# Kernel optimization log

Hardware: AMD Instinct MI355X
Metric: run time of the kernel (lower is better)

Reference implementation:

```python
import jax, jax.numpy as jnp
import numpy as np

D_MODEL = 1024
N_HEADS = 16
B, T = 2, 2048


def setup_inputs() -> dict:
    key = jax.random.key(0)
    ks = jax.random.split(key, 5)
    scale = 1.0 / np.sqrt(D_MODEL)
    return {
        "x": jax.random.normal(ks[0], (B, T, D_MODEL), dtype=jnp.float32),
        "W_q": jax.random.normal(ks[1], (D_MODEL, D_MODEL), dtype=jnp.float32) * scale,
        "W_k": jax.random.normal(ks[2], (D_MODEL, D_MODEL), dtype=jnp.float32) * scale,
        "W_v": jax.random.normal(ks[3], (D_MODEL, D_MODEL), dtype=jnp.float32) * scale,
        "W_o": jax.random.normal(ks[4], (D_MODEL, D_MODEL), dtype=jnp.float32) * scale,
    }


def reference(x, W_q, W_k, W_v, W_o):
    Bn, Tn, D = x.shape
    H = N_HEADS
    Dh = D // H
    # nn.Linear(x) = x @ W.T ; weights stored as [out, in]
    q = (x @ W_q.T).reshape(Bn, Tn, H, Dh).transpose(0, 2, 1, 3)  # [B,H,T,Dh]
    k = (x @ W_k.T).reshape(Bn, Tn, H, Dh).transpose(0, 2, 1, 3)
    v = (x @ W_v.T).reshape(Bn, Tn, H, Dh).transpose(0, 2, 1, 3)
    scores = jnp.einsum("bhqd,bhkd->bhqk", q, k) / np.sqrt(Dh).astype(np.float32)
    attn = jax.nn.softmax(scores, axis=-1)  # [B,H,T,T]
    out = jnp.einsum("bhqk,bhkd->bhqd", attn, v)  # [B,H,T,Dh]
    out = out.transpose(0, 2, 1, 3).reshape(Bn, Tn, D)
    return out @ W_o.T
```

## Files before the change

### kernel.cpp

```cpp
#include <hip/hip_runtime.h>
#include <stdint.h>
#include <stddef.h>


typedef __bf16  bf16x8  __attribute__((ext_vector_type(8)));
typedef __bf16  bf16x4  __attribute__((ext_vector_type(4)));
typedef float   floatx4 __attribute__((ext_vector_type(4)));

#define DEV static __device__ __forceinline__

DEV void ld_g2l16(const void* g, void* l) {
    __builtin_amdgcn_global_load_lds(
        (__attribute__((address_space(1))) void*)g,
        (__attribute__((address_space(3))) void*)l,
        16, 0, 0);
}

#define WK_SCALE 0.18033688011112042f

__global__ __launch_bounds__(256) void cvt_all(
    const float* __restrict__ x,
    const float* __restrict__ wq, const float* __restrict__ wk,
    const float* __restrict__ wv, const float* __restrict__ wo,
    __bf16* __restrict__ xb,
    __bf16* __restrict__ wqb, __bf16* __restrict__ wkb,
    __bf16* __restrict__ wvb, __bf16* __restrict__ wob)
{
    const unsigned t0 = blockIdx.x * 256u + threadIdx.x;
#pragma unroll
    for (int k = 0; k < 4; ++k) {
        unsigned u = t0 + (unsigned)k * 524288u;
        const float* src;
        __bf16* dst;
        unsigned off;
        float mul = 1.0f;
        if (u < 1048576u) {
            src = x; dst = xb; off = u;
        } else {
            unsigned u2 = u - 1048576u;
            unsigned sel = u2 >> 18;
            off = u2 & 0x3FFFFu;
            src = (sel == 0) ? wq : (sel == 1) ? wk : (sel == 2) ? wv : wo;
            dst = (sel == 0) ? wqb : (sel == 1) ? wkb : (sel == 2) ? wvb : wob;
            if (sel == 1) mul = WK_SCALE;
        }
        float4 f = *(const float4*)(src + (size_t)off * 4);
        bf16x4 o = { (__bf16)(f.x * mul), (__bf16)(f.y * mul),
                     (__bf16)(f.z * mul), (__bf16)(f.w * mul) };
        *(bf16x4*)(dst + (size_t)off * 4) = o;
    }
}

template<int BM, int NMAT, bool OUT_F32, bool TR_V, int KH>
__global__ __launch_bounds__(256) void gemm_bt(
    const __bf16* __restrict__ A,
    const __bf16* __restrict__ B0, const __bf16* __restrict__ B1,
    const __bf16* __restrict__ B2,
    void* __restrict__ C0, void* __restrict__ C1, void* __restrict__ C2)
{
    constexpr int Kd = 1024;
    constexpr int N  = 1024;
    constexpr int MI = BM / 32;
    constexpr int NA = BM / 64;
    __shared__ __bf16 As[KH][BM * 32];
    __shared__ __bf16 Bs[KH][128 * 32];

    const int t    = threadIdx.x;
    const int wid  = __builtin_amdgcn_readfirstlane(t >> 6);
    const int lane = t & 63;
    const int quad = lane >> 4;
    const int l15  = lane & 15;

    const int bx  = blockIdx.x;
    const int mat = (NMAT > 1) ? (bx >> 3) : 0;
    const int bn  = (NMAT > 1) ? (bx & 7)  : bx;
    const int bm  = blockIdx.y;
    const __bf16* Bm = (mat == 0) ? B0 : (mat == 1) ? B1 : B2;

    const __bf16* pA[NA];
    const __bf16* pB[2];
#pragma unroll
    for (int i = 0; i < NA; ++i) {
        int c    = i * 256 + t;
        int row  = c >> 2;
        int g    = (c & 3) ^ ((row >> 1) & 3);
        pA[i] = A + (size_t)(bm * BM + row) * Kd + g * 8;
    }
#pragma unroll
    for (int i = 0; i < 2; ++i) {
        int c    = i * 256 + t;
        int row  = c >> 2;
        int g    = (c & 3) ^ ((row >> 1) & 3);
        pB[i] = Bm + (size_t)(bn * 128 + row) * Kd + g * 8;
    }

    const int wm = wid >> 1;
    const int wn = wid & 1;
    const int slotr = quad ^ ((l15 >> 1) & 3);

    floatx4 acc[MI][4];
    const floatx4 z = { 0.f, 0.f, 0.f, 0.f };
#pragma unroll
    for (int i = 0; i < MI; ++i)
#pragma unroll
        for (int j = 0; j < 4; ++j) acc[i][j] = z;

    for (int kb = 0; kb < Kd; kb += 32 * KH) {
        __syncthreads();
#pragma unroll
        for (int h = 0; h < KH; ++h) {
#pragma unroll
            for (int i = 0; i < NA; ++i)
                ld_g2l16(pA[i] + kb + h * 32,
                         (char*)&As[h][0] + i * 4096 + wid * 1024);
#pragma unroll
            for (int i = 0; i < 2; ++i)
                ld_g2l16(pB[i] + kb + h * 32,
                         (char*)&Bs[h][0] + i * 4096 + wid * 1024);
        }
        __syncthreads();

#pragma unroll
        for (int h = 0; h < KH; ++h) {
            bf16x8 af[MI], bf[4];
#pragma unroll
            for (int i = 0; i < MI; ++i) {
                int rowA = wm * (BM / 2) + i * 16 + l15;
                af[i] = *(const bf16x8*)&As[h][rowA * 32 + slotr * 8];
            }
#pragma unroll
            for (int j = 0; j < 4; ++j) {
                int rowB = wn * 64 + j * 16 + l15;
                bf[j] = *(const bf16x8*)&Bs[h][rowB * 32 + slotr * 8];
            }
#pragma unroll
            for (int i = 0; i < MI; ++i)
#pragma unroll
                for (int j = 0; j < 4; ++j)
                    acc[i][j] = __builtin_amdgcn_mfma_f32_16x16x32_bf16(
                        af[i], bf[j], acc[i][j], 0, 0, 0);
        }
    }

    const int row0 = bm * BM + wm * (BM / 2);
    const int col0 = bn * 128 + wn * 64;

    if (TR_V && mat == 2) {
        __bf16* Vt = (__bf16*)C2;
        const int bq    = bm >> 4;
        const int tloc0 = (row0 & 2047) + quad * 4;
#pragma unroll
        for (int i = 0; i < MI; ++i)
#pragma unroll
            for (int j = 0; j < 4; ++j) {
                int col = col0 + j * 16 + l15;
                int hh  = col >> 6, dh = col & 63;
                bf16x4 v = { (__bf16)acc[i][j][0], (__bf16)acc[i][j][1],
                             (__bf16)acc[i][j][2], (__bf16)acc[i][j][3] };
                *(bf16x4*)(Vt + ((size_t)(bq * 16 + hh) * 64 + dh) * 2048
                              + tloc0 + i * 16) = v;
            }
    } else {
        void* Cv = (mat == 0) ? C0 : (mat == 1) ? C1 : C2;
#pragma unroll
        for (int i = 0; i < MI; ++i)
#pragma unroll
            for (int j = 0; j < 4; ++j)
#pragma unroll
                for (int r = 0; r < 4; ++r) {
                    int grow = row0 + i * 16 + quad * 4 + r;
                    int gcol = col0 + j * 16 + l15;
                    if (OUT_F32)
                        ((float*)Cv)[(size_t)grow * N + gcol] = acc[i][j][r];
                    else
                        ((__bf16*)Cv)[(size_t)grow * N + gcol] =
                            (__bf16)acc[i][j][r];
                }
    }
}

__global__ __launch_bounds__(256, 2) void flash_kernel(
    const __bf16* __restrict__ Q, const __bf16* __restrict__ K,
    const __bf16* __restrict__ Vt, __bf16* __restrict__ O)
{
    __shared__ __bf16 Qs[128 * 64];
    __shared__ __bf16 Ks[2][64 * 64];
    __shared__ __bf16 Vs[2][64 * 64];

    const int t    = threadIdx.x;
    const int wid  = __builtin_amdgcn_readfirstlane(t >> 6);
    const int half = wid >> 1;
    const int wsub = wid & 1;
    const int lane = t & 63;
    const int quad = lane >> 4;
    const int l15  = lane & 15;
    const int flat = blockIdx.y * 16 + blockIdx.x;
    const int swz  = (flat & 7) * 64 + (flat >> 3);
    const int qt   = swz & 15;
    const int bh   = swz >> 4;
    const int b    = bh >> 4, h = bh & 15;

#pragma unroll
    for (int i = 0; i < 4; ++i) {
        int c = i * 256 + t;
        int row = c >> 3;
        int g   = (c & 7) ^ (row & 7);
        ld_g2l16(Q + (size_t)(b * 2048 + qt * 128 + row) * 1024 + h * 64 + g * 8,
                 (char*)Qs + i * 4096 + wid * 1024);
    }

    const __bf16* pK[2];
    const __bf16* pV[2];
#pragma unroll
    for (int i = 0; i < 2; ++i) {
        int c = i * 256 + t;
        int srow = c >> 3;
        int sg   = (c & 7) ^ (srow & 7);
        pK[i] = K  + (size_t)(b * 2048 + srow) * 1024 + h * 64 + sg * 8;
        pV[i] = Vt + (size_t)(bh * 64 + srow) * 2048 + sg * 8;
    }

    __syncthreads();

    bf16x8 qf[4][2];
#pragma unroll
    for (int nb = 0; nb < 4; ++nb)
#pragma unroll
        for (int ks = 0; ks < 2; ++ks) {
            int row  = wsub * 64 + nb * 16 + l15;
            int slot = (ks * 4 + quad) ^ (row & 7);
            qf[nb][ks] = *(const bf16x8*)&Qs[row * 64 + slot * 8];
        }

    int koff[2];
#pragma unroll
    for (int ks = 0; ks < 2; ++ks)
        koff[ks] = l15 * 128 + (((ks * 4 + quad) ^ (l15 & 7)) << 4);
    int voff[4];
#pragma unroll
    for (int k16 = 0; k16 < 4; ++k16)
        voff[k16] = l15 * 128 + (((k16 * 2 + (quad >> 1)) ^ (l15 & 7)) << 4)
                  + (quad & 1) * 8;

    const floatx4 z = { 0.f, 0.f, 0.f, 0.f };
    floatx4 o[4][4];
#pragma unroll
    for (int nb = 0; nb < 4; ++nb)
#pragma unroll
        for (int nd = 0; nd < 4; ++nd) o[nb][nd] = z;
    float lsum[4] = { 0.f, 0.f, 0.f, 0.f };

    for (int it = 0; it < 16; ++it) {
        __syncthreads();
#pragma unroll
        for (int i = 0; i < 2; ++i) {
            ld_g2l16(pK[i] + (size_t)it * 65536,
                     (char*)Ks[0] + i * 4096 + wid * 1024);
            ld_g2l16(pK[i] + (size_t)(16 + it) * 65536,
                     (char*)Ks[1] + i * 4096 + wid * 1024);
            ld_g2l16(pV[i] + it * 64,
                     (char*)Vs[0] + i * 4096 + wid * 1024);
            ld_g2l16(pV[i] + (16 + it) * 64,
                     (char*)Vs[1] + i * 4096 + wid * 1024);
        }
        __syncthreads();

        const char* kbase = (const char*)Ks[half];
        const char* vbase = (const char*)Vs[half];
#pragma unroll
        for (int kt32 = 0; kt32 < 2; ++kt32) {
            floatx4 s[2][4];
#pragma unroll
            for (int sub = 0; sub < 2; ++sub) {
#pragma unroll
                for (int nb = 0; nb < 4; ++nb) s[sub][nb] = z;
                const int kt16 = kt32 * 2 + sub;
#pragma unroll
                for (int ks = 0; ks < 2; ++ks) {
                    bf16x8 kf = *(const bf16x8*)(kbase + kt16 * 2048
                                                 + koff[ks]);
#pragma unroll
                    for (int nb = 0; nb < 4; ++nb)
                        s[sub][nb] = __builtin_amdgcn_mfma_f32_16x16x32_bf16(
                            kf, qf[nb][ks], s[sub][nb], 0, 0, 0);
                }
            }
            bf16x8 pb8[4];
#pragma unroll
            for (int nb = 0; nb < 4; ++nb) {
#pragma unroll
                for (int sub = 0; sub < 2; ++sub) {
                    float p0 = __builtin_amdgcn_exp2f(s[sub][nb][0]);
                    float p1 = __builtin_amdgcn_exp2f(s[sub][nb][1]);
                    float p2 = __builtin_amdgcn_exp2f(s[sub][nb][2]);
                    float p3 = __builtin_amdgcn_exp2f(s[sub][nb][3]);
                    lsum[nb] += (p0 + p1) + (p2 + p3);
                    pb8[nb][sub * 4 + 0] = (__bf16)p0;
                    pb8[nb][sub * 4 + 1] = (__bf16)p1;
                    pb8[nb][sub * 4 + 2] = (__bf16)p2;
                    pb8[nb][sub * 4 + 3] = (__bf16)p3;
                }
            }
#pragma unroll
            for (int nd = 0; nd < 4; ++nd) {
                bf16x4 va0 = *(const bf16x4*)(vbase + nd * 2048
                                              + voff[kt32 * 2 + 0]);
                bf16x4 va1 = *(const bf16x4*)(vbase + nd * 2048
                                              + voff[kt32 * 2 + 1]);
                bf16x8 va8;
#pragma unroll
                for (int r = 0; r < 4; ++r) {
                    va8[r]     = va0[r];
                    va8[4 + r] = va1[r];
                }
#pragma unroll
                for (int nb = 0; nb < 4; ++nb)
                    o[nb][nd] = __builtin_amdgcn_mfma_f32_16x16x32_bf16(
                        va8, pb8[nb], o[nb][nd], 0, 0, 0);
            }
        }
    }

    __syncthreads();
    float* obuf = (wsub == 0) ? (float*)&Ks[0][0] : (float*)&Vs[0][0];
    float* lbuf = (float*)&Qs[0] + wsub * 256;
    if (half == 1) {
#pragma unroll
        for (int nb = 0; nb < 4; ++nb)
#pragma unroll
            for (int nd = 0; nd < 4; ++nd)
                *(floatx4*)(obuf + (nb * 4 + nd) * 256 + lane * 4) = o[nb][nd];
#pragma unroll
        for (int nb = 0; nb < 4; ++nb) lbuf[nb * 64 + lane] = lsum[nb];
    }
    __syncthreads();
    if (half == 0) {
#pragma unroll
        for (int nb = 0; nb < 4; ++nb)
#pragma unroll
            for (int nd = 0; nd < 4; ++nd)
                o[nb][nd] += *(const floatx4*)(obuf + (nb * 4 + nd) * 256
                                               + lane * 4);
#pragma unroll
        for (int nb = 0; nb < 4; ++nb) {
            lsum[nb] += lbuf[nb * 64 + lane];
            lsum[nb] += __shfl_xor(lsum[nb], 16);
            lsum[nb] += __shfl_xor(lsum[nb], 32);
        }
#pragma unroll
        for (int nb = 0; nb < 4; ++nb) {
            float inv = 1.f / lsum[nb];
            int token = qt * 128 + wsub * 64 + nb * 16 + l15;
#pragma unroll
            for (int nd = 0; nd < 4; ++nd) {
                bf16x4 ov = { (__bf16)(o[nb][nd][0] * inv),
                              (__bf16)(o[nb][nd][1] * inv),
                              (__bf16)(o[nb][nd][2] * inv),
                              (__bf16)(o[nb][nd][3] * inv) };
                *(bf16x4*)(O + (size_t)(b * 2048 + token) * 1024
                             + h * 64 + nd * 16 + quad * 4) = ov;
            }
        }
    }
}

extern "C" void kernel_launch(void* const* d_in, const int* in_sizes, int n_in,
                              void* d_out, int out_size, void* d_ws, size_t ws_size,
                              hipStream_t stream)
{
    const float* x  = (const float*)d_in[0];
    const float* wq = (const float*)d_in[1];
    const float* wk = (const float*)d_in[2];
    const float* wv = (const float*)d_in[3];
    const float* wo = (const float*)d_in[4];

    char* ws = (char*)d_ws;
    __bf16* xb  = (__bf16*)(ws + 0);
    __bf16* wqb = (__bf16*)(ws + 8388608);
    __bf16* wkb = (__bf16*)(ws + 10485760);
    __bf16* wvb = (__bf16*)(ws + 12582912);
    __bf16* wob = (__bf16*)(ws + 14680064);
    __bf16* Qb  = (__bf16*)(ws + 16777216);
    __bf16* Kb  = (__bf16*)(ws + 25165824);
    __bf16* Vtb = (__bf16*)(ws + 33554432);
    __bf16* Ob  = xb;

    cvt_all<<<2048, 256, 0, stream>>>(x, wq, wk, wv, wo, xb, wqb, wkb, wvb, wob);

    gemm_bt<128, 3, false, true, 1><<<dim3(24, 32), 256, 0, stream>>>(
        xb, wqb, wkb, wvb, (void*)Qb, (void*)Kb, (void*)Vtb);

    flash_kernel<<<dim3(16, 32), 256, 0, stream>>>(Qb, Kb, Vtb, Ob);

    gemm_bt<64, 1, true, false, 2><<<dim3(8, 64), 256, 0, stream>>>(
        Ob, wob, nullptr, nullptr, d_out, nullptr, nullptr);
}
```

Before: 170.7 us.

## Load K and V fragments directly from global memory instead of LDS staging

The flash attention kernel drops the shared-memory staging of K and V tiles and the two block-wide barriers per iteration. Each wave now reads its MFMA K and V fragments straight from global memory through per-lane pointers that advance each iteration. A dedicated float buffer replaces the old K/V arrays for the final cross-half reduction. This removes barriers and LDS traffic, but the two waves sharing a half now load the same K/V data redundantly, and the global reads are less coalesced and rely on cache hits.

```diff
diff --git a/kernel.cpp b/kernel.cpp
--- a/kernel.cpp
+++ b/kernel.cpp
@@ -184,8 +184,7 @@
     const __bf16* __restrict__ Vt, __bf16* __restrict__ O)
 {
     __shared__ __bf16 Qs[128 * 64];
-    __shared__ __bf16 Ks[2][64 * 64];
-    __shared__ __bf16 Vs[2][64 * 64];
+    __shared__ float  mob[2][4096];
 
     const int t    = threadIdx.x;
     const int wid  = __builtin_amdgcn_readfirstlane(t >> 6);
@@ -209,16 +208,10 @@
                  (char*)Qs + i * 4096 + wid * 1024);
     }
 
-    const __bf16* pK[2];
-    const __bf16* pV[2];
-#pragma unroll
-    for (int i = 0; i < 2; ++i) {
-        int c = i * 256 + t;
-        int srow = c >> 3;
-        int sg   = (c & 7) ^ (srow & 7);
-        pK[i] = K  + (size_t)(b * 2048 + srow) * 1024 + h * 64 + sg * 8;
-        pV[i] = Vt + (size_t)(bh * 64 + srow) * 2048 + sg * 8;
-    }
+    const __bf16* pKit = K + (size_t)(b * 2048 + half * 1024 + l15) * 1024
+                           + h * 64 + quad * 8;
+    const __bf16* pVit = Vt + (size_t)(bh * 64 + l15) * 2048
+                            + half * 1024 + quad * 4;
 
     __syncthreads();
 
@@ -232,16 +225,6 @@
             qf[nb][ks] = *(const bf16x8*)&Qs[row * 64 + slot * 8];
         }
 
-    int koff[2];
-#pragma unroll
-    for (int ks = 0; ks < 2; ++ks)
-        koff[ks] = l15 * 128 + (((ks * 4 + quad) ^ (l15 & 7)) << 4);
-    int voff[4];
-#pragma unroll
-    for (int k16 = 0; k16 < 4; ++k16)
-        voff[k16] = l15 * 128 + (((k16 * 2 + (quad >> 1)) ^ (l15 & 7)) << 4)
-                  + (quad & 1) * 8;
-
     const floatx4 z = { 0.f, 0.f, 0.f, 0.f };
     floatx4 o[4][4];
 #pragma unroll
@@ -251,22 +234,6 @@
     float lsum[4] = { 0.f, 0.f, 0.f, 0.f };
 
     for (int it = 0; it < 16; ++it) {
-        __syncthreads();
-#pragma unroll
-        for (int i = 0; i < 2; ++i) {
-            ld_g2l16(pK[i] + (size_t)it * 65536,
-                     (char*)Ks[0] + i * 4096 + wid * 1024);
-            ld_g2l16(pK[i] + (size_t)(16 + it) * 65536,
-                     (char*)Ks[1] + i * 4096 + wid * 1024);
-            ld_g2l16(pV[i] + it * 64,
-                     (char*)Vs[0] + i * 4096 + wid * 1024);
-            ld_g2l16(pV[i] + (16 + it) * 64,
-                     (char*)Vs[1] + i * 4096 + wid * 1024);
-        }
-        __syncthreads();
-
-        const char* kbase = (const char*)Ks[half];
-        const char* vbase = (const char*)Vs[half];
 #pragma unroll
         for (int kt32 = 0; kt32 < 2; ++kt32) {
             floatx4 s[2][4];
@@ -277,8 +244,8 @@
                 const int kt16 = kt32 * 2 + sub;
 #pragma unroll
                 for (int ks = 0; ks < 2; ++ks) {
-                    bf16x8 kf = *(const bf16x8*)(kbase + kt16 * 2048
-                                                 + koff[ks]);
+                    bf16x8 kf = *(const bf16x8*)(pKit
+                                   + (size_t)(kt16 * 16) * 1024 + ks * 32);
 #pragma unroll
                     for (int nb = 0; nb < 4; ++nb)
                         s[sub][nb] = __builtin_amdgcn_mfma_f32_16x16x32_bf16(
@@ -303,10 +270,9 @@
             }
 #pragma unroll
             for (int nd = 0; nd < 4; ++nd) {
-                bf16x4 va0 = *(const bf16x4*)(vbase + nd * 2048
-                                              + voff[kt32 * 2 + 0]);
-                bf16x4 va1 = *(const bf16x4*)(vbase + nd * 2048
-                                              + voff[kt32 * 2 + 1]);
+                const __bf16* pv = pVit + (size_t)(nd * 16) * 2048 + kt32 * 32;
+                bf16x4 va0 = *(const bf16x4*)(pv);
+                bf16x4 va1 = *(const bf16x4*)(pv + 16);
                 bf16x8 va8;
 #pragma unroll
                 for (int r = 0; r < 4; ++r) {
@@ -319,10 +285,12 @@
                         va8, pb8[nb], o[nb][nd], 0, 0, 0);
             }
         }
+        pKit += 64 * 1024;
+        pVit += 64;
     }
 
     __syncthreads();
-    float* obuf = (wsub == 0) ? (float*)&Ks[0][0] : (float*)&Vs[0][0];
+    float* obuf = &mob[wsub][0];
     float* lbuf = (float*)&Qs[0] + wsub * 256;
     if (half == 1) {
 #pragma unroll
```

After: 222.4 us. 1.3x slower.
